# Kernel optimization log

Measured on AMD Instinct MI355X. Metric: run time of the kernel, lower is better.

The kernel has to match this reference:

```python
import jax, jax.numpy as jnp
import numpy as np

N, K, D, H, L = 20000, 32, 256, 8, 3  # nodes, in-degree, d_model, heads, layers
DH = D // H
SCALE = 1.0 / float(np.sqrt(DH))


def setup_inputs() -> dict:
    key = jax.random.key(0)
    ks = jax.random.split(key, 16)
    p = lambda k, shape: jax.random.normal(k, shape, dtype=jnp.float32) * 0.02
    return dict(
        h=jax.random.normal(ks[0], (N, D), dtype=jnp.float32),
        e=jax.random.normal(ks[1], (N, K, D), dtype=jnp.float32),
        src_idx=jax.random.randint(ks[2], (N, K), 0, N),
        in_proj_w=p(ks[3], (L, 3 * D, D)),
        in_proj_b=p(ks[4], (L, 3 * D)),
        out_w=p(ks[5], (L, D, D)),
        out_b=p(ks[6], (L, D)),
        ff1_w=p(ks[7], (L, D, D)),  # dim_feedforward == d_model in this module
        ff1_b=p(ks[8], (L, D)),
        ff2_w=p(ks[9], (L, D, D)),
        ff2_b=p(ks[10], (L, D)),
        ln1_g=jnp.ones((L, D), jnp.float32),
        ln1_b=jnp.zeros((L, D), jnp.float32),
        ln2_g=jnp.ones((L, D), jnp.float32),
        ln2_b=jnp.zeros((L, D), jnp.float32),
    )


def _layernorm(x, g, b):
    mu = x.mean(-1, keepdims=True)
    var = ((x - mu) ** 2).mean(-1, keepdims=True)
    return (x - mu) * jax.lax.rsqrt(var + 1e-5) * g + b


def _mha(x, wqkv, bqkv, wo, bo):
    # x: [N, K, D]; torch packed in_proj: qkv = x @ wqkv.T + bqkv
    n, k, _ = x.shape
    qkv = jnp.einsum('nkd,ed->nke', x, wqkv) + bqkv
    q, kk, v = jnp.split(qkv, 3, axis=-1)
    q = q.reshape(n, k, H, DH)
    kk = kk.reshape(n, k, H, DH)
    v = v.reshape(n, k, H, DH)
    scores = jnp.einsum('nqhc,nkhc->nhqk', q, kk) * SCALE
    attn = jax.nn.softmax(scores, axis=-1)
    out = jnp.einsum('nhqk,nkhc->nqhc', attn, v).reshape(n, k, D)
    return jnp.einsum('nkd,od->nko', out, wo) + bo


def _encoder(x, in_proj_w, in_proj_b, out_w, out_b, ff1_w, ff1_b, ff2_w, ff2_b,
             ln1_g, ln1_b, ln2_g, ln2_b):
    # PyTorch post-norm TransformerEncoderLayer, relu activation, dropout=eval
    for i in range(L):
        a = _mha(x, in_proj_w[i], in_proj_b[i], out_w[i], out_b[i])
        x = _layernorm(x + a, ln1_g[i], ln1_b[i])
        f = jnp.einsum('nkd,od->nko',
                       jax.nn.relu(jnp.einsum('nkd,od->nko', x, ff1_w[i]) + ff1_b[i]),
                       ff2_w[i]) + ff2_b[i]
        x = _layernorm(x + f, ln2_g[i], ln2_b[i])
    return x


def reference(h, e, src_idx, in_proj_w, in_proj_b, out_w, out_b,
              ff1_w, ff1_b, ff2_w, ff2_b, ln1_g, ln1_b, ln2_g, ln2_b):
    # message_func: h_e = h[src] + e  -> mailbox [N, K, D]
    msgs = h[src_idx] + e
    y = _encoder(msgs, in_proj_w, in_proj_b, out_w, out_b,
                 ff1_w, ff1_b, ff2_w, ff2_b, ln1_g, ln1_b, ln2_g, ln2_b)
    # reduce_func: transformer output at position 0 (readout concat is dead code upstream)
    return y[:, 0, :]
```

## Files before the change

kernel.cpp:

```cpp
#include <hip/hip_runtime.h>


#define TOK 32
#define DIM 256
#define NHEAD 8
#define NLAYER 3
#define SCALE 0.17677669529663687f

typedef __bf16 bf16;
typedef __bf16 bf16x8 __attribute__((ext_vector_type(8)));
typedef __bf16 bf16x4 __attribute__((ext_vector_type(4)));
typedef float f32x4 __attribute__((ext_vector_type(4)));

#define MFMA(a, b, c) __builtin_amdgcn_mfma_f32_16x16x32_bf16(a, b, c, 0, 0, 0)

#define OFF_WQKV 0
#define OFF_WO   589824
#define OFF_W1   786432
#define OFF_W2   983040
#define WTOT     1179648

__device__ __forceinline__ float wred_max16(float v) {
  v = fmaxf(v, __shfl_xor(v, 1)); v = fmaxf(v, __shfl_xor(v, 2));
  v = fmaxf(v, __shfl_xor(v, 4)); v = fmaxf(v, __shfl_xor(v, 8));
  return v;
}
__device__ __forceinline__ float wred_sum16(float v) {
  v += __shfl_xor(v, 1); v += __shfl_xor(v, 2);
  v += __shfl_xor(v, 4); v += __shfl_xor(v, 8);
  return v;
}

template <bool AF32, int NT>
__device__ __forceinline__ void gemm_run(const float* Af, const bf16* Ab,
                                         const bf16* __restrict__ W, int obase,
                                         int quad, int lc, int mtiles, int qlim,
                                         f32x4 (&acc)[2][NT]) {
#pragma unroll
  for (int m = 0; m < 2; m++)
#pragma unroll
    for (int j = 0; j < NT; j++) acc[m][j] = (f32x4){0.f, 0.f, 0.f, 0.f};

  auto loadA = [&](int m0, int k0) -> bf16x8 {
    const int row = m0 + lc;
    const int col = k0 + quad * 8;
    if constexpr (AF32) {
      const f32x4* p = (const f32x4*)(Af + row * 260 + col);
      f32x4 x0 = p[0];
      f32x4 x1 = p[1];
      bf16x8 r;
      r[0] = (bf16)x0[0]; r[1] = (bf16)x0[1]; r[2] = (bf16)x0[2]; r[3] = (bf16)x0[3];
      r[4] = (bf16)x1[0]; r[5] = (bf16)x1[1]; r[6] = (bf16)x1[2]; r[7] = (bf16)x1[3];
      return r;
    } else {
      return *(const bf16x8*)(Ab + row * 264 + col);
    }
  };
  auto loadB = [&](int j, int k0) -> bf16x8 {
    return *(const bf16x8*)(W + (obase + j * 16 + lc) * DIM + k0 + quad * 8);
  };

  bf16x8 a0 = loadA(0, 0);
  bf16x8 a1 = loadA(16, 0);
  bf16x8 b[NT];
#pragma unroll
  for (int j = 0; j < NT; j++) b[j] = loadB(j, 0);

#pragma unroll
  for (int ks = 0; ks < 8; ks++) {
    bf16x8 na0, na1, nb[NT];
    if (ks < 7) {
      na0 = loadA(0, (ks + 1) * 32);
      na1 = loadA(16, (ks + 1) * 32);
#pragma unroll
      for (int j = 0; j < NT; j++) nb[j] = loadB(j, (ks + 1) * 32);
    }
#pragma unroll
    for (int j = 0; j < NT; j++) {
      acc[0][j] = MFMA(a0, b[j], acc[0][j]);
      if (mtiles > 1 && (qlim == 0 || (obase + j * 16) >= qlim))
        acc[1][j] = MFMA(a1, b[j], acc[1][j]);
    }
    a0 = na0; a1 = na1;
#pragma unroll
    for (int j = 0; j < NT; j++) b[j] = nb[j];
  }
}

__device__ __forceinline__ void lnorm(float (*xf)[260], const float* __restrict__ g,
                                      const float* __restrict__ b, int tid) {
  const int t = tid >> 4, i = tid & 15;
  float v[16];
  float s = 0.f;
#pragma unroll
  for (int j = 0; j < 16; j++) { v[j] = xf[t][i + 16 * j]; s += v[j]; }
  s = wred_sum16(s);
  const float mu = s * (1.f / 256.f);
  float q = 0.f;
#pragma unroll
  for (int j = 0; j < 16; j++) { const float d = v[j] - mu; q += d * d; }
  q = wred_sum16(q);
  const float inv = rsqrtf(q * (1.f / 256.f) + 1e-5f);
#pragma unroll
  for (int j = 0; j < 16; j++) {
    const int d = i + 16 * j;
    xf[t][d] = (v[j] - mu) * inv * g[d] + b[d];
  }
}

__global__ __launch_bounds__(256) void cvtw(const float* __restrict__ wq,
                                            const float* __restrict__ wo,
                                            const float* __restrict__ w1,
                                            const float* __restrict__ w2,
                                            bf16* __restrict__ ws) {
  const int i = (blockIdx.x * 256 + threadIdx.x) * 4;
  float4 v;
  if (i < OFF_WO)       v = *(const float4*)(wq + i);
  else if (i < OFF_W1)  v = *(const float4*)(wo + (i - OFF_WO));
  else if (i < OFF_W2)  v = *(const float4*)(w1 + (i - OFF_W1));
  else                  v = *(const float4*)(w2 + (i - OFF_W2));
  bf16x4 r;
  r[0] = (bf16)v.x; r[1] = (bf16)v.y; r[2] = (bf16)v.z; r[3] = (bf16)v.w;
  *(bf16x4*)(ws + i) = r;
}

__global__ __launch_bounds__(512, 2) void nt_fused(
    const float* __restrict__ h, const float* __restrict__ e, const int* __restrict__ src,
    const bf16* __restrict__ wall, const float* __restrict__ inb,
    const float* __restrict__ outbias, const float* __restrict__ f1b,
    const float* __restrict__ f2b, const float* __restrict__ l1g,
    const float* __restrict__ l1b, const float* __restrict__ l2g,
    const float* __restrict__ l2b, float* __restrict__ out) {
  __shared__ float xf[TOK][260];
  __shared__ bf16 qb[TOK][264];
  __shared__ bf16 kb[TOK][264];
  __shared__ bf16 vt[DIM][40];
  __shared__ bf16 ob[TOK][264];
  __shared__ bf16 pb[NHEAD][TOK][40];

  const int node = blockIdx.x;
  const int tid = threadIdx.x;
  const int wave = tid >> 6;
  const int lane = tid & 63;
  const int quad = lane >> 4;
  const int lc = lane & 15;

  {
    const int t = tid >> 4;
    const int i = tid & 15;
    const int s = src[node * TOK + t];
    const float* hp = h + (size_t)s * DIM + i * 16;
    const float* ep = e + ((size_t)node * TOK + t) * DIM + i * 16;
#pragma unroll
    for (int j = 0; j < 4; j++) {
      const f32x4 hv = *(const f32x4*)(hp + 4 * j);
      const f32x4 ev = *(const f32x4*)(ep + 4 * j);
      *(f32x4*)&xf[t][i * 16 + 4 * j] = hv + ev;
    }
  }
  __syncthreads();

#pragma unroll 1
  for (int layer = 0; layer < NLAYER; layer++) {
    const bool lastl = (layer == NLAYER - 1);
    const bf16* Wq = wall + OFF_WQKV + layer * (768 * 256);
    const bf16* Wo = wall + OFF_WO + layer * 65536;
    const bf16* W1 = wall + OFF_W1 + layer * 65536;
    const bf16* W2 = wall + OFF_W2 + layer * 65536;
    const float* bq = inb + layer * 768;
    const float* bo = outbias + layer * 256;
    const float* b1 = f1b + layer * 256;
    const float* b2 = f2b + layer * 256;
    const float* g1 = l1g + layer * 256;
    const float* be1 = l1b + layer * 256;
    const float* g2 = l2g + layer * 256;
    const float* be2 = l2b + layer * 256;

    {
      f32x4 acc[2][6];
      gemm_run<true, 6>(&xf[0][0], nullptr, Wq, wave * 96, quad, lc, 2,
                        lastl ? 256 : 0, acc);
#pragma unroll
      for (int j = 0; j < 6; j++) {
        const int o = wave * 96 + j * 16 + lc;
        const float bias = bq[o];
#pragma unroll
        for (int m = 0; m < 2; m++) {
#pragma unroll
          for (int r = 0; r < 4; r++) {
            const int t = m * 16 + quad * 4 + r;
            const float v = acc[m][j][r] + bias;
            if (o < 256)      qb[t][o] = (bf16)v;
            else if (o < 512) kb[t][o - 256] = (bf16)v;
            else              vt[o - 512][t] = (bf16)v;
          }
        }
      }
    }
    __syncthreads();

    {
      const int hh = wave;
      const int nT = lastl ? 1 : 2;
      const f32x4 z4 = {0.f, 0.f, 0.f, 0.f};
      bf16x8 aq[2], bk[2];
#pragma unroll
      for (int ti = 0; ti < 2; ti++)
        if (ti < nT) aq[ti] = *(const bf16x8*)&qb[ti * 16 + lc][hh * 32 + quad * 8];
#pragma unroll
      for (int ui = 0; ui < 2; ui++)
        bk[ui] = *(const bf16x8*)&kb[ui * 16 + lc][hh * 32 + quad * 8];
      f32x4 sA[2][2];
#pragma unroll
      for (int ti = 0; ti < 2; ti++)
        if (ti < nT) {
          sA[ti][0] = MFMA(aq[ti], bk[0], z4);
          sA[ti][1] = MFMA(aq[ti], bk[1], z4);
        }
#pragma unroll
      for (int ti = 0; ti < 2; ti++)
        if (ti < nT) {
#pragma unroll
          for (int r = 0; r < 4; r++) {
            float p0 = sA[ti][0][r] * SCALE;
            float p1 = sA[ti][1][r] * SCALE;
            const float mx = wred_max16(fmaxf(p0, p1));
            p0 = __expf(p0 - mx);
            p1 = __expf(p1 - mx);
            const float rs = 1.f / wred_sum16(p0 + p1);
            const int t = ti * 16 + quad * 4 + r;
            pb[hh][t][lc] = (bf16)(p0 * rs);
            pb[hh][t][16 + lc] = (bf16)(p1 * rs);
          }
        }
      bf16x8 ap[2], bv[2];
#pragma unroll
      for (int ti = 0; ti < 2; ti++)
        if (ti < nT) ap[ti] = *(const bf16x8*)&pb[hh][ti * 16 + lc][quad * 8];
#pragma unroll
      for (int ci = 0; ci < 2; ci++)
        bv[ci] = *(const bf16x8*)&vt[hh * 32 + ci * 16 + lc][quad * 8];
#pragma unroll
      for (int ti = 0; ti < 2; ti++)
        if (ti < nT) {
#pragma unroll
          for (int ci = 0; ci < 2; ci++) {
            const f32x4 oo = MFMA(ap[ti], bv[ci], z4);
#pragma unroll
            for (int r = 0; r < 4; r++)
              ob[ti * 16 + quad * 4 + r][hh * 32 + ci * 16 + lc] = (bf16)oo[r];
          }
        }
    }
    __syncthreads();

    {
      const int mt = lastl ? 1 : 2;
      f32x4 acc[2][2];
      gemm_run<false, 2>(nullptr, &ob[0][0], Wo, wave * 32, quad, lc, mt, 0, acc);
#pragma unroll
      for (int j = 0; j < 2; j++) {
        const int o = wave * 32 + j * 16 + lc;
        const float bias = bo[o];
#pragma unroll
        for (int m = 0; m < 2; m++)
          if (m < mt) {
#pragma unroll
            for (int r = 0; r < 4; r++) {
              const int t = m * 16 + quad * 4 + r;
              xf[t][o] += acc[m][j][r] + bias;
            }
          }
      }
    }
    __syncthreads();
    lnorm(xf, g1, be1, tid);
    __syncthreads();

    {
      const int mt = lastl ? 1 : 2;
      f32x4 acc[2][2];
      gemm_run<true, 2>(&xf[0][0], nullptr, W1, wave * 32, quad, lc, mt, 0, acc);
#pragma unroll
      for (int j = 0; j < 2; j++) {
        const int o = wave * 32 + j * 16 + lc;
        const float bias = b1[o];
#pragma unroll
        for (int m = 0; m < 2; m++)
          if (m < mt) {
#pragma unroll
            for (int r = 0; r < 4; r++) {
              const int t = m * 16 + quad * 4 + r;
              ob[t][o] = (bf16)fmaxf(acc[m][j][r] + bias, 0.f);
            }
          }
      }
    }
    __syncthreads();

    {
      const int mt = lastl ? 1 : 2;
      f32x4 acc[2][2];
      gemm_run<false, 2>(nullptr, &ob[0][0], W2, wave * 32, quad, lc, mt, 0, acc);
#pragma unroll
      for (int j = 0; j < 2; j++) {
        const int o = wave * 32 + j * 16 + lc;
        const float bias = b2[o];
#pragma unroll
        for (int m = 0; m < 2; m++)
          if (m < mt) {
#pragma unroll
            for (int r = 0; r < 4; r++) {
              const int t = m * 16 + quad * 4 + r;
              xf[t][o] += acc[m][j][r] + bias;
            }
          }
      }
    }
    __syncthreads();
    lnorm(xf, g2, be2, tid);
    __syncthreads();
  }

  if (tid < 64) {
    *(f32x4*)(out + (size_t)node * DIM + tid * 4) = *(const f32x4*)&xf[0][tid * 4];
  }
}

extern "C" void kernel_launch(void* const* d_in, const int* in_sizes, int n_in,
                              void* d_out, int out_size, void* d_ws, size_t ws_size,
                              hipStream_t stream) {
  (void)in_sizes; (void)n_in; (void)out_size; (void)ws_size;
  const float* h   = (const float*)d_in[0];
  const float* e   = (const float*)d_in[1];
  const int* src   = (const int*)d_in[2];
  const float* inw = (const float*)d_in[3];
  const float* inb = (const float*)d_in[4];
  const float* ow  = (const float*)d_in[5];
  const float* obi = (const float*)d_in[6];
  const float* f1w = (const float*)d_in[7];
  const float* f1b = (const float*)d_in[8];
  const float* f2w = (const float*)d_in[9];
  const float* f2b = (const float*)d_in[10];
  const float* l1g = (const float*)d_in[11];
  const float* l1b = (const float*)d_in[12];
  const float* l2g = (const float*)d_in[13];
  const float* l2b = (const float*)d_in[14];
  bf16* ws = (bf16*)d_ws;

  cvtw<<<1152, 256, 0, stream>>>(inw, ow, f1w, f2w, ws);
  nt_fused<<<20000, 512, 0, stream>>>(h, e, src, ws, inb, obi, f1b, f2b,
                                      l1g, l1b, l2g, l2b, (float*)d_out);
}
```

Baseline: 8.071 ms.

## Store residual in bf16 LDS and reuse buffers to raise occupancy

The residual stream moves from an fp32 LDS buffer to bf16, and the probability and attention-output scratch buffers are folded into the qb and kb buffers. This shrinks shared memory per block enough to raise the launch bound from 2 to 4 blocks per CU. The GEMM drops its explicit register double-buffering and the fp32-to-bf16 conversion on A loads, and layernorm switches to vectorised accesses. The cost is lower accuracy in the residual and layernorm path, plus less software prefetching of loads, and it leaves a dead loop in the gather code.

Result: slower. 8.366 ms (+3.7%).

```diff
diff --git a/kernel.cpp b/kernel.cpp
--- a/kernel.cpp
+++ b/kernel.cpp
@@ -6,6 +6,7 @@
 #define NHEAD 8
 #define NLAYER 3
 #define SCALE 0.17677669529663687f
+#define XS 264
 
 typedef __bf16 bf16;
 typedef __bf16 bf16x8 __attribute__((ext_vector_type(8)));
@@ -31,8 +32,8 @@
   return v;
 }
 
-template <bool AF32, int NT>
-__device__ __forceinline__ void gemm_run(const float* Af, const bf16* Ab,
+template <int NT>
+__device__ __forceinline__ void gemm_run(const bf16* __restrict__ A,
                                          const bf16* __restrict__ W, int obase,
                                          int quad, int lc, int mtiles, int qlim,
                                          f32x4 (&acc)[2][NT]) {
@@ -41,59 +42,33 @@
 #pragma unroll
     for (int j = 0; j < NT; j++) acc[m][j] = (f32x4){0.f, 0.f, 0.f, 0.f};
 
-  auto loadA = [&](int m0, int k0) -> bf16x8 {
-    const int row = m0 + lc;
-    const int col = k0 + quad * 8;
-    if constexpr (AF32) {
-      const f32x4* p = (const f32x4*)(Af + row * 260 + col);
-      f32x4 x0 = p[0];
-      f32x4 x1 = p[1];
-      bf16x8 r;
-      r[0] = (bf16)x0[0]; r[1] = (bf16)x0[1]; r[2] = (bf16)x0[2]; r[3] = (bf16)x0[3];
-      r[4] = (bf16)x1[0]; r[5] = (bf16)x1[1]; r[6] = (bf16)x1[2]; r[7] = (bf16)x1[3];
-      return r;
-    } else {
-      return *(const bf16x8*)(Ab + row * 264 + col);
-    }
-  };
-  auto loadB = [&](int j, int k0) -> bf16x8 {
-    return *(const bf16x8*)(W + (obase + j * 16 + lc) * DIM + k0 + quad * 8);
-  };
-
-  bf16x8 a0 = loadA(0, 0);
-  bf16x8 a1 = loadA(16, 0);
-  bf16x8 b[NT];
-#pragma unroll
-  for (int j = 0; j < NT; j++) b[j] = loadB(j, 0);
-
 #pragma unroll
   for (int ks = 0; ks < 8; ks++) {
-    bf16x8 na0, na1, nb[NT];
-    if (ks < 7) {
-      na0 = loadA(0, (ks + 1) * 32);
-      na1 = loadA(16, (ks + 1) * 32);
-#pragma unroll
-      for (int j = 0; j < NT; j++) nb[j] = loadB(j, (ks + 1) * 32);
-    }
+    const int kc = ks * 32 + quad * 8;
+    const bf16x8 a0 = *(const bf16x8*)(A + lc * XS + kc);
+    bf16x8 a1;
+    if (mtiles > 1) a1 = *(const bf16x8*)(A + (16 + lc) * XS + kc);
 #pragma unroll
     for (int j = 0; j < NT; j++) {
-      acc[0][j] = MFMA(a0, b[j], acc[0][j]);
+      const bf16x8 b = *(const bf16x8*)(W + (obase + j * 16 + lc) * DIM + kc);
+      acc[0][j] = MFMA(a0, b, acc[0][j]);
       if (mtiles > 1 && (qlim == 0 || (obase + j * 16) >= qlim))
-        acc[1][j] = MFMA(a1, b[j], acc[1][j]);
-    }
-    a0 = na0; a1 = na1;
-#pragma unroll
-    for (int j = 0; j < NT; j++) b[j] = nb[j];
-  }
-}
-
-__device__ __forceinline__ void lnorm(float (*xf)[260], const float* __restrict__ g,
+        acc[1][j] = MFMA(a1, b, acc[1][j]);
+    }
+  }
+}
+
+__device__ __forceinline__ void lnorm(bf16 (*xf)[XS], const float* __restrict__ g,
                                       const float* __restrict__ b, int tid) {
   const int t = tid >> 4, i = tid & 15;
+  const bf16x8 v0 = *(const bf16x8*)&xf[t][i * 16];
+  const bf16x8 v1 = *(const bf16x8*)&xf[t][i * 16 + 8];
   float v[16];
+#pragma unroll
+  for (int j = 0; j < 8; j++) { v[j] = (float)v0[j]; v[8 + j] = (float)v1[j]; }
   float s = 0.f;
 #pragma unroll
-  for (int j = 0; j < 16; j++) { v[j] = xf[t][i + 16 * j]; s += v[j]; }
+  for (int j = 0; j < 16; j++) s += v[j];
   s = wred_sum16(s);
   const float mu = s * (1.f / 256.f);
   float q = 0.f;
@@ -101,11 +76,20 @@
   for (int j = 0; j < 16; j++) { const float d = v[j] - mu; q += d * d; }
   q = wred_sum16(q);
   const float inv = rsqrtf(q * (1.f / 256.f) + 1e-5f);
-#pragma unroll
-  for (int j = 0; j < 16; j++) {
-    const int d = i + 16 * j;
-    xf[t][d] = (v[j] - mu) * inv * g[d] + b[d];
-  }
+  f32x4 gv[4], bv[4];
+#pragma unroll
+  for (int j = 0; j < 4; j++) {
+    gv[j] = *(const f32x4*)(g + i * 16 + 4 * j);
+    bv[j] = *(const f32x4*)(b + i * 16 + 4 * j);
+  }
+  bf16x8 o0, o1;
+#pragma unroll
+  for (int j = 0; j < 8; j++) {
+    o0[j] = (bf16)((v[j] - mu) * inv * gv[j >> 2][j & 3] + bv[j >> 2][j & 3]);
+    o1[j] = (bf16)((v[8 + j] - mu) * inv * gv[2 + (j >> 2)][j & 3] + bv[2 + (j >> 2)][j & 3]);
+  }
+  *(bf16x8*)&xf[t][i * 16] = o0;
+  *(bf16x8*)&xf[t][i * 16 + 8] = o1;
 }
 
 __global__ __launch_bounds__(256) void cvtw(const float* __restrict__ wq,
@@ -124,19 +108,17 @@
   *(bf16x4*)(ws + i) = r;
 }
 
-__global__ __launch_bounds__(512, 2) void nt_fused(
+__global__ __launch_bounds__(512, 4) void nt_fused(
     const float* __restrict__ h, const float* __restrict__ e, const int* __restrict__ src,
     const bf16* __restrict__ wall, const float* __restrict__ inb,
     const float* __restrict__ outbias, const float* __restrict__ f1b,
     const float* __restrict__ f2b, const float* __restrict__ l1g,
     const float* __restrict__ l1b, const float* __restrict__ l2g,
     const float* __restrict__ l2b, float* __restrict__ out) {
-  __shared__ float xf[TOK][260];
-  __shared__ bf16 qb[TOK][264];
-  __shared__ bf16 kb[TOK][264];
-  __shared__ bf16 vt[DIM][40];
-  __shared__ bf16 ob[TOK][264];
-  __shared__ bf16 pb[NHEAD][TOK][40];
+  __shared__ __align__(16) bf16 xf[TOK][XS];
+  __shared__ __align__(16) bf16 qb[TOK][XS];
+  __shared__ __align__(16) bf16 kb[TOK][XS];
+  __shared__ __align__(16) bf16 vt[DIM][40];
 
   const int node = blockIdx.x;
   const int tid = threadIdx.x;
@@ -151,12 +133,26 @@
     const int s = src[node * TOK + t];
     const float* hp = h + (size_t)s * DIM + i * 16;
     const float* ep = e + ((size_t)node * TOK + t) * DIM + i * 16;
+    bf16x8 r0, r1;
+#pragma unroll
+    for (int j = 0; j < 2; j++) {
+      const f32x4 a = *(const f32x4*)(hp + 4 * j) + *(const f32x4*)(ep + 4 * j);
+      const f32x4 b = *(const f32x4*)(hp + 8 + 4 * j) + *(const f32x4*)(ep + 8 + 4 * j);
+      bf16x8& r = j ? r1 : r0;
+      (void)r;
+    }
+    const f32x4 a0 = *(const f32x4*)(hp + 0) + *(const f32x4*)(ep + 0);
+    const f32x4 a1 = *(const f32x4*)(hp + 4) + *(const f32x4*)(ep + 4);
+    const f32x4 a2 = *(const f32x4*)(hp + 8) + *(const f32x4*)(ep + 8);
+    const f32x4 a3 = *(const f32x4*)(hp + 12) + *(const f32x4*)(ep + 12);
+    bf16x8 w0, w1;
 #pragma unroll
     for (int j = 0; j < 4; j++) {
-      const f32x4 hv = *(const f32x4*)(hp + 4 * j);
-      const f32x4 ev = *(const f32x4*)(ep + 4 * j);
-      *(f32x4*)&xf[t][i * 16 + 4 * j] = hv + ev;
-    }
+      w0[j] = (bf16)a0[j]; w0[4 + j] = (bf16)a1[j];
+      w1[j] = (bf16)a2[j]; w1[4 + j] = (bf16)a3[j];
+    }
+    *(bf16x8*)&xf[t][i * 16] = w0;
+    *(bf16x8*)&xf[t][i * 16 + 8] = w1;
   }
   __syncthreads();
 
@@ -178,8 +174,7 @@
 
     {
       f32x4 acc[2][6];
-      gemm_run<true, 6>(&xf[0][0], nullptr, Wq, wave * 96, quad, lc, 2,
-                        lastl ? 256 : 0, acc);
+      gemm_run<6>(&xf[0][0], Wq, wave * 96, quad, lc, 2, lastl ? 256 : 0, acc);
 #pragma unroll
       for (int j = 0; j < 6; j++) {
         const int o = wave * 96 + j * 16 + lc;
@@ -229,14 +224,14 @@
             p1 = __expf(p1 - mx);
             const float rs = 1.f / wred_sum16(p0 + p1);
             const int t = ti * 16 + quad * 4 + r;
-            pb[hh][t][lc] = (bf16)(p0 * rs);
-            pb[hh][t][16 + lc] = (bf16)(p1 * rs);
+            qb[t][hh * 32 + lc] = (bf16)(p0 * rs);
+            qb[t][hh * 32 + 16 + lc] = (bf16)(p1 * rs);
           }
         }
       bf16x8 ap[2], bv[2];
 #pragma unroll
       for (int ti = 0; ti < 2; ti++)
-        if (ti < nT) ap[ti] = *(const bf16x8*)&pb[hh][ti * 16 + lc][quad * 8];
+        if (ti < nT) ap[ti] = *(const bf16x8*)&qb[ti * 16 + lc][hh * 32 + quad * 8];
 #pragma unroll
       for (int ci = 0; ci < 2; ci++)
         bv[ci] = *(const bf16x8*)&vt[hh * 32 + ci * 16 + lc][quad * 8];
@@ -248,7 +243,7 @@
             const f32x4 oo = MFMA(ap[ti], bv[ci], z4);
 #pragma unroll
             for (int r = 0; r < 4; r++)
-              ob[ti * 16 + quad * 4 + r][hh * 32 + ci * 16 + lc] = (bf16)oo[r];
+              kb[ti * 16 + quad * 4 + r][hh * 32 + ci * 16 + lc] = (bf16)oo[r];
           }
         }
     }
@@ -257,7 +252,7 @@
     {
       const int mt = lastl ? 1 : 2;
       f32x4 acc[2][2];
-      gemm_run<false, 2>(nullptr, &ob[0][0], Wo, wave * 32, quad, lc, mt, 0, acc);
+      gemm_run<2>(&kb[0][0], Wo, wave * 32, quad, lc, mt, 0, acc);
 #pragma unroll
       for (int j = 0; j < 2; j++) {
         const int o = wave * 32 + j * 16 + lc;
@@ -268,7 +263,7 @@
 #pragma unroll
             for (int r = 0; r < 4; r++) {
               const int t = m * 16 + quad * 4 + r;
-              xf[t][o] += acc[m][j][r] + bias;
+              xf[t][o] = (bf16)((float)xf[t][o] + acc[m][j][r] + bias);
             }
           }
       }
@@ -280,7 +275,7 @@
     {
       const int mt = lastl ? 1 : 2;
       f32x4 acc[2][2];
-      gemm_run<true, 2>(&xf[0][0], nullptr, W1, wave * 32, quad, lc, mt, 0, acc);
+      gemm_run<2>(&xf[0][0], W1, wave * 32, quad, lc, mt, 0, acc);
 #pragma unroll
       for (int j = 0; j < 2; j++) {
         const int o = wave * 32 + j * 16 + lc;
@@ -291,7 +286,7 @@
 #pragma unroll
             for (int r = 0; r < 4; r++) {
               const int t = m * 16 + quad * 4 + r;
-              ob[t][o] = (bf16)fmaxf(acc[m][j][r] + bias, 0.f);
+              kb[t][o] = (bf16)fmaxf(acc[m][j][r] + bias, 0.f);
             }
           }
       }
@@ -301,7 +296,7 @@
     {
       const int mt = lastl ? 1 : 2;
       f32x4 acc[2][2];
-      gemm_run<false, 2>(nullptr, &ob[0][0], W2, wave * 32, quad, lc, mt, 0, acc);
+      gemm_run<2>(&kb[0][0], W2, wave * 32, quad, lc, mt, 0, acc);
 #pragma unroll
       for (int j = 0; j < 2; j++) {
         const int o = wave * 32 + j * 16 + lc;
@@ -312,7 +307,7 @@
 #pragma unroll
             for (int r = 0; r < 4; r++) {
               const int t = m * 16 + quad * 4 + r;
-              xf[t][o] += acc[m][j][r] + bias;
+              xf[t][o] = (bf16)((float)xf[t][o] + acc[m][j][r] + bias);
             }
           }
       }
@@ -323,7 +318,10 @@
   }
 
   if (tid < 64) {
-    *(f32x4*)(out + (size_t)node * DIM + tid * 4) = *(const f32x4*)&xf[0][tid * 4];
+    const bf16x4 v = *(const bf16x4*)&xf[0][tid * 4];
+    f32x4 o;
+    o[0] = (float)v[0]; o[1] = (float)v[1]; o[2] = (float)v[2]; o[3] = (float)v[3];
+    *(f32x4*)(out + (size_t)node * DIM + tid * 4) = o;
   }
 }
 
```
